# Kernel optimization log

Hardware: AMD Instinct MI355X
Metric: run time of the kernel (lower is better)

The kernel has to match this reference:

```python
import jax, jax.numpy as jnp
import numpy as np

D_MODEL = 1024
NHEAD = 16
HEAD_DIM = D_MODEL // NHEAD
LN_EPS = 1e-5
ROPE_BASE = 10000.0


def _rope_cos_sin(n, head_dim):
    inv_freq = 1.0 / (ROPE_BASE ** (jnp.arange(0, head_dim, 2, dtype=jnp.float32) / head_dim))
    t = jnp.arange(n, dtype=jnp.float32)
    freqs = jnp.outer(t, inv_freq)  # (N, head_dim//2)
    return jnp.cos(freqs), jnp.sin(freqs)


def _apply_rope(x, cos, sin):
    # x: (B, H, N, hd); cos/sin: (N, hd//2)
    B, H, N, hd = x.shape
    xr = x.reshape(B, H, N, hd // 2, 2)
    x0, x1 = xr[..., 0], xr[..., 1]
    c = cos[None, None]
    s = sin[None, None]
    rot = jnp.stack([x0 * c - x1 * s, x0 * s + x1 * c], axis=-1)
    return rot.reshape(B, H, N, hd)


def setup_inputs() -> dict:
    key = jax.random.key(0)
    ks = jax.random.split(key, 6)
    D = D_MODEL
    scale = 1.0 / np.sqrt(D)
    x = jax.random.normal(ks[0], (2, 2048, D), dtype=jnp.float32)
    Wq = jax.random.normal(ks[1], (D, D), dtype=jnp.float32) * scale
    Wk = jax.random.normal(ks[2], (D, D), dtype=jnp.float32) * scale
    Wv = jax.random.normal(ks[3], (D, D), dtype=jnp.float32) * scale
    Wo = jax.random.normal(ks[4], (D, D), dtype=jnp.float32) * scale
    bq = jnp.zeros((D,), jnp.float32)
    bk = jnp.zeros((D,), jnp.float32)
    bv = jnp.zeros((D,), jnp.float32)
    bo = jnp.zeros((D,), jnp.float32)
    ln_w = jnp.ones((D,), jnp.float32)
    ln_b = jnp.zeros((D,), jnp.float32)
    return {"x": x, "ln_w": ln_w, "ln_b": ln_b, "Wq": Wq, "bq": bq,
            "Wk": Wk, "bk": bk, "Wv": Wv, "bv": bv, "Wo": Wo, "bo": bo}


def reference(x, ln_w, ln_b, Wq, bq, Wk, bk, Wv, bv, Wo, bo):
    B, N, D = x.shape
    H, hd = NHEAD, HEAD_DIM
    # LayerNorm
    mu = jnp.mean(x, axis=-1, keepdims=True)
    var = jnp.mean(jnp.square(x - mu), axis=-1, keepdims=True)
    xn = (x - mu) * jax.lax.rsqrt(var + LN_EPS) * ln_w + ln_b
    # QKV projections -> (B, H, N, hd)
    def proj(W, b):
        return (xn @ W.T + b).reshape(B, N, H, hd).transpose(0, 2, 1, 3)
    q = proj(Wq, bq)
    k = proj(Wk, bk)
    v = proj(Wv, bv)
    cos, sin = _rope_cos_sin(N, hd)
    q = _apply_rope(q, cos, sin)
    k = _apply_rope(k, cos, sin)
    scores = jnp.einsum('bhqd,bhkd->bhqk', q, k) / jnp.sqrt(jnp.float32(hd))
    attn = jax.nn.softmax(scores, axis=-1)
    out = jnp.einsum('bhqk,bhkd->bhqd', attn, v)
    out = out.transpose(0, 2, 1, 3).reshape(B, N, D)
    return x + out @ Wo.T + bo
```

## Files before the change

### kernel.cpp

```cpp
#include <hip/hip_runtime.h>


#define SEQ 2048
#define LN_EPS 1e-5f

using short8 = __attribute__((ext_vector_type(8))) short;
using f32x4  = __attribute__((ext_vector_type(4))) float;
using f32x16 = __attribute__((ext_vector_type(16))) float;

__device__ __forceinline__ unsigned short f2bf(float f) {
  union { float f; unsigned u; } v; v.f = f;
  unsigned r = v.u + 0x7FFFu + ((v.u >> 16) & 1u);
  return (unsigned short)(r >> 16);
}

__device__ __forceinline__ void async16(const void* g, void* l) {
  __builtin_amdgcn_global_load_lds(
      (const __attribute__((address_space(1))) void*)g,
      (__attribute__((address_space(3))) void*)l, 16, 0, 0);
}

__global__ __launch_bounds__(256) void prep_kernel(
    const float* __restrict__ x, const float* __restrict__ lnw, const float* __restrict__ lnb,
    const float* __restrict__ wq, const float* __restrict__ wk,
    const float* __restrict__ wv, const float* __restrict__ wo,
    unsigned short* __restrict__ wqkv, unsigned short* __restrict__ wob,
    unsigned short* __restrict__ xn, float2* __restrict__ tab) {
  const int b = blockIdx.x, t = threadIdx.x;
  if (b < 4096) {
    const int gid = b * 256 + t;
    const int m = gid >> 18, e4 = gid & 262143;
    const float* src = (m == 0) ? wq : (m == 1) ? wk : (m == 2) ? wv : wo;
    const float4 v = ((const float4*)src)[e4];
    ushort4 o; o.x = f2bf(v.x); o.y = f2bf(v.y); o.z = f2bf(v.z); o.w = f2bf(v.w);
    if (m < 3) ((ushort4*)wqkv)[(size_t)m * 262144 + e4] = o;
    else       ((ushort4*)wob)[e4] = o;
  } else if (b < 8192) {
    const int row = b - 4096;
    const float4 v = ((const float4*)(x + (size_t)row * 1024))[t];
    float s  = v.x + v.y + v.z + v.w;
    float s2 = v.x * v.x + v.y * v.y + v.z * v.z + v.w * v.w;
#pragma unroll
    for (int off = 32; off >= 1; off >>= 1) {
      s  += __shfl_xor(s, off);
      s2 += __shfl_xor(s2, off);
    }
    __shared__ float red[8];
    const int lane = t & 63, wave = t >> 6;
    if (lane == 0) { red[wave] = s; red[4 + wave] = s2; }
    __syncthreads();
    s  = red[0] + red[1] + red[2] + red[3];
    s2 = red[4] + red[5] + red[6] + red[7];
    const float mu   = s * (1.0f / 1024.0f);
    const float var  = s2 * (1.0f / 1024.0f) - mu * mu;
    const float rstd = rsqrtf(var + LN_EPS);
    const float4 wv4 = ((const float4*)lnw)[t];
    const float4 bv4 = ((const float4*)lnb)[t];
    ushort4 o;
    o.x = f2bf((v.x - mu) * rstd * wv4.x + bv4.x);
    o.y = f2bf((v.y - mu) * rstd * wv4.y + bv4.y);
    o.z = f2bf((v.z - mu) * rstd * wv4.z + bv4.z);
    o.w = f2bf((v.w - mu) * rstd * wv4.w + bv4.w);
    ((ushort4*)xn)[(size_t)row * 256 + t] = o;
  } else {
    const int gid = (b - 8192) * 256 + t;
    const int pos = gid >> 5, ip = gid & 31;
    const float invf = exp2f((float)ip * -0.4152410118609203f);
    const float fr = (float)pos * invf;
    tab[gid] = make_float2(cosf(fr), sinf(fr));
  }
}

__global__ __launch_bounds__(256, 3) void gemm_qkv_kernel(
    const unsigned short* __restrict__ A,
    const unsigned short* __restrict__ Bw,
    const float* __restrict__ bq, const float* __restrict__ bk, const float* __restrict__ bv,
    const float2* __restrict__ tab,
    unsigned short* __restrict__ qb, unsigned short* __restrict__ kbg,
    unsigned short* __restrict__ vtb) {
  __shared__ unsigned short lA[128 * 64];
  __shared__ unsigned short lB[128 * 64];
  const int tid = threadIdx.x;
  const int lane = tid & 63, wave = tid >> 6;
  const int lr = lane & 15, quad = lane >> 4;
  const int wm = (wave >> 1) * 64, wn = (wave & 1) * 64;
  const int n0 = blockIdx.x * 128, m0 = blockIdx.y * 128;
  const int r7 = lr & 7;
  const int lrow = lane >> 3, lcg = (lane & 7) ^ lrow;
  const int lin = blockIdx.y * gridDim.x + blockIdx.x;
  const int phase = ((lin >> 8) * 5) & 15;

  f32x4 acc[4][4];
#pragma unroll
  for (int i = 0; i < 4; ++i)
#pragma unroll
    for (int j = 0; j < 4; ++j) acc[i][j] = (f32x4){0.f, 0.f, 0.f, 0.f};

  for (int kt = 0; kt < 16; ++kt) {
    const int kofs = ((kt + phase) & 15) * 64;
    __syncthreads();
#pragma unroll
    for (int c = 0; c < 4; ++c) {
      const int chunk = wave * 4 + c;
      const int grow = chunk * 8 + lrow;
      async16(&A[(size_t)(m0 + grow) * 1024 + kofs + lcg * 8], &lA[chunk * 512]);
      async16(&Bw[(size_t)(n0 + grow) * 1024 + kofs + lcg * 8], &lB[chunk * 512]);
    }
    __syncthreads();
#pragma unroll
    for (int kk = 0; kk < 2; ++kk) {
      short8 a[4], b[4];
#pragma unroll
      for (int i = 0; i < 4; ++i)
        a[i] = *(const short8*)&lA[(wm + i * 16 + lr) * 64 + ((kk * 4 + quad) ^ r7) * 8];
#pragma unroll
      for (int j = 0; j < 4; ++j)
        b[j] = *(const short8*)&lB[(wn + j * 16 + lr) * 64 + ((kk * 4 + quad) ^ r7) * 8];
#pragma unroll
      for (int i = 0; i < 4; ++i)
#pragma unroll
        for (int j = 0; j < 4; ++j)
          acc[i][j] = __builtin_amdgcn_mfma_f32_16x16x32_bf16(a[i], b[j], acc[i][j], 0, 0, 0);
    }
  }

  const int which = n0 >> 10;
  const float* bias = (which == 0) ? bq : (which == 1) ? bk : bv;
  const float qs = (which == 0) ? 0.18033688011112042f : 1.0f;
#pragma unroll
  for (int i = 0; i < 4; ++i)
#pragma unroll
    for (int j = 0; j < 4; ++j)
#pragma unroll
      for (int r = 0; r < 4; ++r) {
        const int row = m0 + wm + i * 16 + quad * 4 + r;
        const int col = n0 + wn + j * 16 + lr;
        const int c = col & 1023;
        float val = (acc[i][j][r] + bias[c]) * qs;
        const int head = c >> 6, hd_i = c & 63;
        const int b_ = row >> 11, pos = row & 2047;
        if (which < 2) {
          const float partner = __shfl_xor(val, 1);
          const float2 cs = tab[(pos << 5) + (hd_i >> 1)];
          val = val * cs.x + partner * ((lane & 1) ? cs.y : -cs.y);
        }
        if (which == 2) {
          vtb[((size_t)((b_ * 16 + head) * 64 + hd_i)) * SEQ + pos] = f2bf(val);
        } else {
          const size_t didx = ((size_t)((b_ * 16 + head) * SEQ + pos)) * 64 + hd_i;
          if (which == 0) qb[didx] = f2bf(val);
          else            kbg[didx] = f2bf(val);
        }
      }
}

__global__ __launch_bounds__(256, 3) void gemm_o_kernel(
    const unsigned short* __restrict__ A,
    const unsigned short* __restrict__ Bw,
    const float* __restrict__ bo, const float* __restrict__ xres, float* __restrict__ out) {
  __shared__ unsigned short lA[128 * 64];
  __shared__ unsigned short lB[64 * 64];
  const int tid = threadIdx.x;
  const int lane = tid & 63, wave = tid >> 6;
  const int lr = lane & 15, quad = lane >> 4;
  const int wm = (wave >> 1) * 64, wn = (wave & 1) * 32;
  const int n0 = blockIdx.x * 64, m0 = blockIdx.y * 128;
  const int r7 = lr & 7;
  const int lrow = lane >> 3, lcg = (lane & 7) ^ lrow;
  const int lin = blockIdx.y * gridDim.x + blockIdx.x;
  const int phase = ((lin >> 8) * 8) & 15;

  f32x4 acc[4][2];
#pragma unroll
  for (int i = 0; i < 4; ++i)
#pragma unroll
    for (int j = 0; j < 2; ++j) acc[i][j] = (f32x4){0.f, 0.f, 0.f, 0.f};

  for (int kt = 0; kt < 16; ++kt) {
    const int kofs = ((kt + phase) & 15) * 64;
    __syncthreads();
#pragma unroll
    for (int c = 0; c < 4; ++c) {
      const int chunk = wave * 4 + c;
      const int grow = chunk * 8 + lrow;
      async16(&A[(size_t)(m0 + grow) * 1024 + kofs + lcg * 8], &lA[chunk * 512]);
    }
#pragma unroll
    for (int c = 0; c < 2; ++c) {
      const int chunk = wave * 2 + c;
      const int grow = chunk * 8 + lrow;
      async16(&Bw[(size_t)(n0 + grow) * 1024 + kofs + lcg * 8], &lB[chunk * 512]);
    }
    __syncthreads();
#pragma unroll
    for (int kk = 0; kk < 2; ++kk) {
      short8 a[4], b[2];
#pragma unroll
      for (int i = 0; i < 4; ++i)
        a[i] = *(const short8*)&lA[(wm + i * 16 + lr) * 64 + ((kk * 4 + quad) ^ r7) * 8];
#pragma unroll
      for (int j = 0; j < 2; ++j)
        b[j] = *(const short8*)&lB[(wn + j * 16 + lr) * 64 + ((kk * 4 + quad) ^ r7) * 8];
#pragma unroll
      for (int i = 0; i < 4; ++i)
#pragma unroll
        for (int j = 0; j < 2; ++j)
          acc[i][j] = __builtin_amdgcn_mfma_f32_16x16x32_bf16(a[i], b[j], acc[i][j], 0, 0, 0);
    }
  }

#pragma unroll
  for (int i = 0; i < 4; ++i)
#pragma unroll
    for (int j = 0; j < 2; ++j)
#pragma unroll
      for (int r = 0; r < 4; ++r) {
        const int row = m0 + wm + i * 16 + quad * 4 + r;
        const int col = n0 + wn + j * 16 + lr;
        const size_t idx = (size_t)row * 1024 + col;
        out[idx] = acc[i][j][r] + bo[col] + xres[idx];
      }
}

__global__ __launch_bounds__(512, 4) void attn_kernel(
    const unsigned short* __restrict__ qg, const unsigned short* __restrict__ kg,
    const unsigned short* __restrict__ vtg, unsigned short* __restrict__ ao) {
  __shared__ unsigned short lds[32768];
  const int tid = threadIdx.x;
  const int lane = tid & 63, w = tid >> 6;
  const int ws = w & 3, kh = w >> 2;
  const int l31 = lane & 31, hb = lane >> 5;
  const int bh = blockIdx.x >> 4, qt = blockIdx.x & 15;
  const int q0w = qt * 128 + ws * 32;
  const int phase32 = ((blockIdx.x >> 8) & 1) * 16;
  const unsigned short* Q  = qg + (size_t)bh * SEQ * 64;
  const unsigned short* K  = kg + (size_t)bh * SEQ * 64;
  const unsigned short* VT = vtg + (size_t)bh * 64 * SEQ;

  short8 qf[4];
#pragma unroll
  for (int c = 0; c < 4; ++c)
    qf[c] = *(const short8*)&Q[(size_t)(q0w + l31) * 64 + c * 16 + hb * 8];

  f32x16 o[2];
#pragma unroll
  for (int dh = 0; dh < 2; ++dh)
#pragma unroll
    for (int r = 0; r < 16; ++r) o[dh][r] = 0.f;
  float ls = 0.f;

  const int khbase = kh * 1024;
  const int srow_k = ws * 8 + (lane >> 3), gk = lane & 7;
  const int srow_v = ws * 16 + (lane >> 2), gv = lane & 3;
  const unsigned short* Ksrc = K + (size_t)(khbase + srow_k) * 64 + gk * 8;
  const unsigned short* Vsrc = VT + (size_t)srow_v * SEQ + khbase + gv * 8;
  const int kds = (gk * 32 + (srow_k ^ gk)) * 8;
  const int g2s = gv * 2 + (srow_v >> 5);
  const int vds = (g2s * 32 + ((srow_v & 31) ^ g2s)) * 8;
  unsigned short* const base_kh = lds + kh * 4096;

  int koff[4], voff[2][2];
#pragma unroll
  for (int c = 0; c < 4; ++c) {
    const int fk = c * 2 + hb;
    koff[c] = (fk * 32 + (l31 ^ fk)) * 8;
  }
#pragma unroll
  for (int cl = 0; cl < 2; ++cl)
#pragma unroll
    for (int dh = 0; dh < 2; ++dh) {
      const int f = (cl * 2 + hb) * 2 + dh;
      voff[cl][dh] = 2048 + (f * 32 + (l31 ^ f)) * 8;
    }

  auto TILE = [&](const unsigned short* Tb) {
    f32x16 sv;
#pragma unroll
    for (int r = 0; r < 16; ++r) sv[r] = 0.f;
    __builtin_amdgcn_s_setprio(1);
#pragma unroll
    for (int c = 0; c < 4; ++c) {
      const short8 af = *(const short8*)&Tb[koff[c]];
      sv = __builtin_amdgcn_mfma_f32_32x32x16_bf16(af, qf[c], sv, 0, 0, 0);
    }
    __builtin_amdgcn_s_setprio(0);
    unsigned wp[8];
#pragma unroll
    for (int p = 0; p < 8; ++p) {
      union { float f; unsigned u; } e0, e1;
      e0.f = __builtin_amdgcn_exp2f(sv[2 * p]);
      e1.f = __builtin_amdgcn_exp2f(sv[2 * p + 1]);
      ls += e0.f + e1.f;
      wp[p] = __builtin_amdgcn_perm(e1.u, e0.u, 0x07060302u);
    }
    unsigned wlo[8], whi[8];
#pragma unroll
    for (int p = 0; p < 8; ++p) {
      auto rr = __builtin_amdgcn_permlane32_swap(wp[p], wp[p], false, false);
      wlo[p] = rr[0]; whi[p] = rr[1];
    }
    __builtin_amdgcn_s_setprio(1);
#pragma unroll
    for (int cl = 0; cl < 2; ++cl) {
      const int pb = cl * 4;
      union { unsigned u[4]; short8 s; } pf;
      pf.u[0] = hb ? wlo[pb + 2] : wlo[pb + 0];
      pf.u[1] = hb ? wlo[pb + 3] : wlo[pb + 1];
      pf.u[2] = hb ? whi[pb + 2] : whi[pb + 0];
      pf.u[3] = hb ? whi[pb + 3] : whi[pb + 1];
#pragma unroll
      for (int dh = 0; dh < 2; ++dh) {
        const short8 vf = *(const short8*)&Tb[voff[cl][dh]];
        o[dh] = __builtin_amdgcn_mfma_f32_32x32x16_bf16(pf.s, vf, o[dh], 0, 0, 0);
      }
    }
    __builtin_amdgcn_s_setprio(0);
  };

#pragma unroll
  for (int j = 0; j < 2; ++j) {
    const int tl = (j + phase32) & 31;
    const short8 R0 = *(const short8*)(Ksrc + (size_t)tl * 2048);
    const short8 R2 = *(const short8*)(Vsrc + tl * 32);
    *(short8*)(base_kh + j * 8192 + kds) = R0;
    *(short8*)(base_kh + j * 8192 + 2048 + vds) = R2;
  }
  __syncthreads();

  for (int it = 0; it < 16; ++it) {
    const int cs = (it & 1) * 2;
    const int ss = cs ^ 2;
    short8 R0, R2;
    if (it < 15) {
      const int tl = (2 * it + 2 + phase32) & 31;
      R0 = *(const short8*)(Ksrc + (size_t)tl * 2048);
      R2 = *(const short8*)(Vsrc + tl * 32);
    }
    TILE(base_kh + cs * 8192);
    if (it < 15) {
      *(short8*)(base_kh + ss * 8192 + kds) = R0;
      *(short8*)(base_kh + ss * 8192 + 2048 + vds) = R2;
      const int tl = (2 * it + 3 + phase32) & 31;
      R0 = *(const short8*)(Ksrc + (size_t)tl * 2048);
      R2 = *(const short8*)(Vsrc + tl * 32);
    }
    TILE(base_kh + (cs + 1) * 8192);
    if (it < 15) {
      *(short8*)(base_kh + (ss + 1) * 8192 + kds) = R0;
      *(short8*)(base_kh + (ss + 1) * 8192 + 2048 + vds) = R2;
    }
    __syncthreads();
  }

  union { float f; unsigned u; } lsu; lsu.f = ls;
  auto lr2 = __builtin_amdgcn_permlane32_swap(lsu.u, lsu.u, false, false);
  union { unsigned u; float f; } la, lb2; la.u = lr2[0]; lb2.u = lr2[1];
  const float lsH = la.f + lb2.f;

  float* osh = (float*)lds;
  float* lsh = (float*)(lds + 16384);
  if (kh == 1) {
#pragma unroll
    for (int dh = 0; dh < 2; ++dh)
#pragma unroll
      for (int r = 0; r < 16; ++r)
        osh[((ws * 2 + dh) * 16 + r) * 64 + lane] = o[dh][r];
    lsh[ws * 64 + lane] = lsH;
  }
  __syncthreads();
  if (kh == 0) {
    const float rl = 1.0f / (lsH + lsh[ws * 64 + lane]);
    const int b_ = bh >> 4, h = bh & 15;
#pragma unroll
    for (int r = 0; r < 16; ++r) {
      const int m = (r & 3) + 8 * (r >> 2) + 4 * hb;
      const float rlv = __shfl(rl, m);
      const int row = q0w + m;
#pragma unroll
      for (int dh = 0; dh < 2; ++dh) {
        const float ov = o[dh][r] + osh[((ws * 2 + dh) * 16 + r) * 64 + lane];
        ao[(size_t)(b_ * SEQ + row) * 1024 + h * 64 + dh * 32 + l31] = f2bf(ov * rlv);
      }
    }
  }
}

extern "C" void kernel_launch(void* const* d_in, const int* in_sizes, int n_in,
                              void* d_out, int out_size, void* d_ws, size_t ws_size,
                              hipStream_t stream) {
  const float* x   = (const float*)d_in[0];
  const float* lnw = (const float*)d_in[1];
  const float* lnb = (const float*)d_in[2];
  const float* Wq  = (const float*)d_in[3];
  const float* bq  = (const float*)d_in[4];
  const float* Wk  = (const float*)d_in[5];
  const float* bk  = (const float*)d_in[6];
  const float* Wv  = (const float*)d_in[7];
  const float* bv  = (const float*)d_in[8];
  const float* Wo  = (const float*)d_in[9];
  const float* bo  = (const float*)d_in[10];
  float* out = (float*)d_out;

  char* ws = (char*)d_ws;
  unsigned short* wqkv = (unsigned short*)(ws);
  unsigned short* wob  = (unsigned short*)(ws + 6291456);
  unsigned short* xn   = (unsigned short*)(ws + 8388608);
  unsigned short* qb   = (unsigned short*)(ws + 16777216);
  unsigned short* kbuf = (unsigned short*)(ws + 25165824);
  unsigned short* vtb  = (unsigned short*)(ws + 33554432);
  unsigned short* ao   = (unsigned short*)(ws + 41943040);
  float2*         tab  = (float2*)(ws + 50331648);

  hipLaunchKernelGGL(prep_kernel, dim3(8448), dim3(256), 0, stream,
                     x, lnw, lnb, Wq, Wk, Wv, Wo, wqkv, wob, xn, tab);
  hipLaunchKernelGGL(gemm_qkv_kernel, dim3(24, 32), dim3(256), 0, stream,
                     xn, wqkv, bq, bk, bv, tab, qb, kbuf, vtb);
  hipLaunchKernelGGL(attn_kernel, dim3(512), dim3(512), 0, stream, qb, kbuf, vtb, ao);
  hipLaunchKernelGGL(gemm_o_kernel, dim3(16, 32), dim3(256), 0, stream,
                     ao, wob, bo, x, out);
}
```

Before: 207.2 us.

## Prefetch GEMM tiles into registers to overlap global loads with MFMA

Both the QKV and output-projection GEMMs replace the direct global-to-LDS async loads with register-staged prefetch. The next K tile is loaded into registers while the MFMAs run on the current tile, then written to LDS between barriers. This is meant to hide global memory latency behind compute in a single-buffered LDS scheme. It costs extra registers, so the output GEMM's occupancy hint drops from 3 to 2 blocks per SM, and each iteration still takes two barriers.

Result: no change. 209.6 us (+1.2%).

```diff
diff --git a/kernel.cpp b/kernel.cpp
--- a/kernel.cpp
+++ b/kernel.cpp
@@ -12,12 +12,6 @@
   union { float f; unsigned u; } v; v.f = f;
   unsigned r = v.u + 0x7FFFu + ((v.u >> 16) & 1u);
   return (unsigned short)(r >> 16);
-}
-
-__device__ __forceinline__ void async16(const void* g, void* l) {
-  __builtin_amdgcn_global_load_lds(
-      (const __attribute__((address_space(1))) void*)g,
-      (__attribute__((address_space(3))) void*)l, 16, 0, 0);
 }
 
 __global__ __launch_bounds__(256) void prep_kernel(
@@ -96,17 +90,31 @@
 #pragma unroll
     for (int j = 0; j < 4; ++j) acc[i][j] = (f32x4){0.f, 0.f, 0.f, 0.f};
 
+  const unsigned short* Asrc = A + (size_t)(m0 + (wave * 4) * 8 + lrow) * 1024 + lcg * 8;
+  const unsigned short* Bsrc = Bw + (size_t)(n0 + (wave * 4) * 8 + lrow) * 1024 + lcg * 8;
+  short8 RA[4], RB[4];
+
+#define QKV_ISSUE(kt_) {                                                   \
+    const int kofs = (((kt_) + phase) & 15) * 64;                          \
+    _Pragma("unroll")                                                      \
+    for (int c = 0; c < 4; ++c) {                                          \
+      RA[c] = *(const short8*)(Asrc + (size_t)c * 8 * 1024 + kofs);        \
+      RB[c] = *(const short8*)(Bsrc + (size_t)c * 8 * 1024 + kofs);        \
+    }                                                                      \
+  }
+#define QKV_WRITE() {                                                      \
+    _Pragma("unroll")                                                      \
+    for (int c = 0; c < 4; ++c) {                                          \
+      *(short8*)&lA[(wave * 4 + c) * 512 + lane * 8] = RA[c];              \
+      *(short8*)&lB[(wave * 4 + c) * 512 + lane * 8] = RB[c];              \
+    }                                                                      \
+  }
+
+  QKV_ISSUE(0); QKV_WRITE();
+  __syncthreads();
+
   for (int kt = 0; kt < 16; ++kt) {
-    const int kofs = ((kt + phase) & 15) * 64;
-    __syncthreads();
-#pragma unroll
-    for (int c = 0; c < 4; ++c) {
-      const int chunk = wave * 4 + c;
-      const int grow = chunk * 8 + lrow;
-      async16(&A[(size_t)(m0 + grow) * 1024 + kofs + lcg * 8], &lA[chunk * 512]);
-      async16(&Bw[(size_t)(n0 + grow) * 1024 + kofs + lcg * 8], &lB[chunk * 512]);
-    }
-    __syncthreads();
+    if (kt < 15) QKV_ISSUE(kt + 1);
 #pragma unroll
     for (int kk = 0; kk < 2; ++kk) {
       short8 a[4], b[4];
@@ -121,6 +129,11 @@
 #pragma unroll
         for (int j = 0; j < 4; ++j)
           acc[i][j] = __builtin_amdgcn_mfma_f32_16x16x32_bf16(a[i], b[j], acc[i][j], 0, 0, 0);
+    }
+    if (kt < 15) {
+      __syncthreads();
+      QKV_WRITE();
+      __syncthreads();
     }
   }
 
@@ -154,7 +167,7 @@
       }
 }
 
-__global__ __launch_bounds__(256, 3) void gemm_o_kernel(
+__global__ __launch_bounds__(256, 2) void gemm_o_kernel(
     const unsigned short* __restrict__ A,
     const unsigned short* __restrict__ Bw,
     const float* __restrict__ bo, const float* __restrict__ xres, float* __restrict__ out) {
@@ -176,22 +189,33 @@
 #pragma unroll
     for (int j = 0; j < 2; ++j) acc[i][j] = (f32x4){0.f, 0.f, 0.f, 0.f};
 
+  const unsigned short* Asrc = A + (size_t)(m0 + (wave * 4) * 8 + lrow) * 1024 + lcg * 8;
+  const unsigned short* Bsrc = Bw + (size_t)(n0 + (wave * 2) * 8 + lrow) * 1024 + lcg * 8;
+  short8 RA[4], RB[2];
+
+#define O_ISSUE(kt_) {                                                     \
+    const int kofs = (((kt_) + phase) & 15) * 64;                          \
+    _Pragma("unroll")                                                      \
+    for (int c = 0; c < 4; ++c)                                            \
+      RA[c] = *(const short8*)(Asrc + (size_t)c * 8 * 1024 + kofs);        \
+    _Pragma("unroll")                                                      \
+    for (int c = 0; c < 2; ++c)                                            \
+      RB[c] = *(const short8*)(Bsrc + (size_t)c * 8 * 1024 + kofs);        \
+  }
+#define O_WRITE() {                                                        \
+    _Pragma("unroll")                                                      \
+    for (int c = 0; c < 4; ++c)                                            \
+      *(short8*)&lA[(wave * 4 + c) * 512 + lane * 8] = RA[c];              \
+    _Pragma("unroll")                                                      \
+    for (int c = 0; c < 2; ++c)                                            \
+      *(short8*)&lB[(wave * 2 + c) * 512 + lane * 8] = RB[c];              \
+  }
+
+  O_ISSUE(0); O_WRITE();
+  __syncthreads();
+
   for (int kt = 0; kt < 16; ++kt) {
-    const int kofs = ((kt + phase) & 15) * 64;
-    __syncthreads();
-#pragma unroll
-    for (int c = 0; c < 4; ++c) {
-      const int chunk = wave * 4 + c;
-      const int grow = chunk * 8 + lrow;
-      async16(&A[(size_t)(m0 + grow) * 1024 + kofs + lcg * 8], &lA[chunk * 512]);
-    }
-#pragma unroll
-    for (int c = 0; c < 2; ++c) {
-      const int chunk = wave * 2 + c;
-      const int grow = chunk * 8 + lrow;
-      async16(&Bw[(size_t)(n0 + grow) * 1024 + kofs + lcg * 8], &lB[chunk * 512]);
-    }
-    __syncthreads();
+    if (kt < 15) O_ISSUE(kt + 1);
 #pragma unroll
     for (int kk = 0; kk < 2; ++kk) {
       short8 a[4], b[2];
@@ -206,6 +230,11 @@
 #pragma unroll
         for (int j = 0; j < 2; ++j)
           acc[i][j] = __builtin_amdgcn_mfma_f32_16x16x32_bf16(a[i], b[j], acc[i][j], 0, 0, 0);
+    }
+    if (kt < 15) {
+      __syncthreads();
+      O_WRITE();
+      __syncthreads();
     }
   }
 
```
